# Optimization experiments

Measured on AMD Instinct MI355X. Metric: run time of the kernel, lower is better.

## Reference

```python
import jax, jax.numpy as jnp
import numpy as np

T, B, D, H, MID, A = 512, 128, 256, 512, 512, 3


def setup_inputs() -> dict:
    key = jax.random.key(0)
    ks = jax.random.split(key, 16)
    kb = 1.0 / np.sqrt(H)

    def u(kk, shape):
        return jax.random.uniform(kk, shape, jnp.float32, -kb, kb)

    def lin(kk, fan_in, fan_out, std=0.05):
        k1, k2 = jax.random.split(kk)
        return (jax.random.normal(k1, (fan_out, fan_in), jnp.float32) * std,
                jnp.full((fan_out,), 1e-6, jnp.float32))

    aw0, ab0 = lin(ks[6], H + D, MID)
    aw1, ab1 = lin(ks[7], MID, MID)
    aw2, ab2 = lin(ks[8], MID, A, std=0.1 / np.sqrt(MID))
    cw0, cb0 = lin(ks[9], H + D, MID)
    cw1, cb1 = lin(ks[10], MID, MID)
    cw2, cb2 = lin(ks[11], MID, 1, std=0.5 / np.sqrt(MID))

    return {
        "state": jax.random.normal(ks[0], (T, B, D), jnp.float32),
        "hidden_state": jnp.zeros((B, H), jnp.float32),
        "cell_state": jnp.zeros((B, H), jnp.float32),
        "len_sequence": jax.random.randint(ks[1], (B,), 1, T + 1),
        "W_ih": u(ks[2], (4 * H, D)), "W_hh": u(ks[3], (4 * H, H)),
        "b_ih": u(ks[4], (4 * H,)), "b_hh": u(ks[5], (4 * H,)),
        "aw0": aw0, "ab0": ab0, "aw1": aw1, "ab1": ab1, "aw2": aw2, "ab2": ab2,
        "cw0": cw0, "cb0": cb0, "cw1": cw1, "cb1": cb1, "cw2": cw2, "cb2": cb2,
    }


def _pack_indices(len_sequence):
    # ragged packing: concat first len[b] timesteps of each batch row
    lens = np.asarray(len_sequence)
    return jnp.asarray(np.concatenate(
        [b * T + np.arange(l) for b, l in enumerate(lens)]))


def _mlp(x, w0, b0, w1, b1, w2, b2):
    h = jax.nn.relu(x @ w0.T + b0)
    h = jax.nn.relu(h @ w1.T + b1)
    return h @ w2.T + b2


def reference(state, hidden_state, cell_state, len_sequence,
              W_ih, W_hh, b_ih, b_hh,
              aw0, ab0, aw1, ab1, aw2, ab2,
              cw0, cb0, cw1, cb1, cw2, cb2):
    flat_idx = _pack_indices(len_sequence)

    def step(carry, x_t):
        h, c = carry
        gates = x_t @ W_ih.T + b_ih + h @ W_hh.T + b_hh
        i, f, g, o = jnp.split(gates, 4, axis=-1)
        c = jax.nn.sigmoid(f) * c + jax.nn.sigmoid(i) * jnp.tanh(g)
        h = jax.nn.sigmoid(o) * jnp.tanh(c)
        return (h, c), h

    _, hs = jax.lax.scan(step, (hidden_state, cell_state), state)  # [T,B,H]

    rnn_emb = hs.transpose(1, 0, 2).reshape(B * T, H)[flat_idx]      # [N,H]
    st = state.transpose(1, 0, 2).reshape(B * T, D)[flat_idx]        # [N,D]
    inp = jnp.concatenate([st, rnn_emb], axis=1)                     # [N,D+H]

    actor = jnp.tanh(_mlp(inp, aw0, ab0, aw1, ab1, aw2, ab2))
    critic = _mlp(inp, cw0, cb0, cw1, cb1, cw2, cb2)
    return actor, critic
```

## Files before the change

### kernel.cpp

```cpp
#include <hip/hip_runtime.h>
#include <stdint.h>


#define T_STEPS 512
#define BATCH   128
#define DDIM    256
#define HDIM    512

typedef __attribute__((ext_vector_type(8))) short bf16x8;
typedef __attribute__((ext_vector_type(4))) float f32x4;
typedef __attribute__((ext_vector_type(2))) unsigned long long u64x2;
typedef unsigned short u16;
typedef unsigned int   u32;
typedef unsigned long long u64;
typedef __attribute__((ext_vector_type(4))) u32 u32x4;

__device__ __forceinline__ u16 f2bf(float x){
  u32 u = __builtin_bit_cast(u32, x);
  u32 r = u + 0x7fffu + ((u >> 16) & 1u);
  return (u16)(r >> 16);
}
__device__ __forceinline__ float bf2f(u16 h){
  u32 u = ((u32)h) << 16;
  return __builtin_bit_cast(float, u);
}
__device__ __forceinline__ float sigm(float x){ return 1.f/(1.f + __expf(-x)); }
__device__ __forceinline__ float tanh_f(float x){ return 1.f - 2.f/(1.f + __expf(2.f*x)); }

__device__ __forceinline__ void async_ld16(const void* g, void* l){
  __builtin_amdgcn_global_load_lds(
      (const __attribute__((address_space(1))) u32*)g,
      (__attribute__((address_space(3))) u32*)l, 16, 0, 0);
}

__device__ __forceinline__ void ld2_b128_cc_issue(const void* p0, const void* p1,
                                                  u32x4& A0, u32x4& A1){
  asm volatile("global_load_dwordx4 %0, %2, off sc0 sc1\n\t"
               "global_load_dwordx4 %1, %3, off sc0 sc1"
               : "=&v"(A0), "=&v"(A1) : "v"(p0), "v"(p1) : "memory");
}

__global__ void sniff_kernel(const u16* __restrict__ b, int* __restrict__ mode){
  if (threadIdx.x == 0){
    int bad = 0;
    for (int i = 0; i < 64; i++){
      u16 x = b[2*i];
      int e = (x >> 7) & 0xFF;
      if (e < 0x60 || e > 0x85) bad++;
    }
    *mode = (bad > 16) ? 1 : 0;
  }
}

__global__ void cvt_kernel(const void* __restrict__ src, u16* __restrict__ dst,
                           int n, const int* __restrict__ mode){
  int i0 = (blockIdx.x*blockDim.x + threadIdx.x) * 8;
  if (i0 >= n) return;
  int m = *mode;
  if (m){
    const float* s = (const float*)src;
    if (i0 + 8 <= n){
      float4 a = *(const float4*)(s + i0);
      float4 b = *(const float4*)(s + i0 + 4);
      ushort4 oa, ob;
      oa.x=f2bf(a.x); oa.y=f2bf(a.y); oa.z=f2bf(a.z); oa.w=f2bf(a.w);
      ob.x=f2bf(b.x); ob.y=f2bf(b.y); ob.z=f2bf(b.z); ob.w=f2bf(b.w);
      *(ushort4*)(dst + i0) = oa;
      *(ushort4*)(dst + i0 + 4) = ob;
    } else {
      for (int i = i0; i < n; i++) dst[i] = f2bf(s[i]);
    }
  } else {
    const u16* s = (const u16*)src;
    if (i0 + 8 <= n){
      *(ushort4*)(dst + i0)     = *(const ushort4*)(s + i0);
      *(ushort4*)(dst + i0 + 4) = *(const ushort4*)(s + i0 + 4);
    } else {
      for (int i = i0; i < n; i++) dst[i] = s[i];
    }
  }
}

__global__ void scan_kernel(const int* __restrict__ lens, int* __restrict__ off){
  if (threadIdx.x == 0){
    int a = 0;
    for (int b = 0; b < BATCH; b++){ off[b] = a; a += lens[b]; }
    off[BATCH] = a;
  }
}

__global__ void pack_state_kernel(const u16* __restrict__ st_bf,
                                  const int* __restrict__ lens,
                                  const int* __restrict__ off,
                                  u16* __restrict__ inp){
  int r = blockIdx.x*4 + (threadIdx.x >> 6);
  int lane = threadIdx.x & 63;
  int b = r & (BATCH-1), t = r >> 7;
  if (t >= lens[b]) return;
  long row = (long)off[b] + t;
  ushort4 v = ((const ushort4*)(st_bf + (long)r*DDIM))[lane];
  ((ushort4*)(inp + row*768))[lane] = v;
}

__global__ void zero_out_kernel(void* __restrict__ out, int n,
                                const int* __restrict__ mode){
  int i = blockIdx.x*blockDim.x + threadIdx.x;
  if (i >= n) return;
  if (*mode) ((float*)out)[i] = 0.f; else ((u16*)out)[i] = 0;
}

__global__ __launch_bounds__(512, 1) void lstm_kernel(
    const u16* __restrict__ Whh, const u16* __restrict__ Wih,
    const u16* __restrict__ bih, const u16* __restrict__ bhh,
    const u16* __restrict__ cell0,
    const u16* __restrict__ state,
    u16* hbuf,
    u16* __restrict__ inp,
    const int* __restrict__ off, const int* __restrict__ lens,
    int* tags)
{
  const int tid  = threadIdx.x;
  const int wave = tid >> 6;
  const int lane = tid & 63;
  const int g    = blockIdx.x >> 4;
  const int s    = blockIdx.x & 15;
  const int Sb   = s * 32;
  const int q    = lane >> 4;
  const int m16  = lane & 15;

  __shared__ u16  wlds[65536];
  __shared__ u16  hlds[8192];
  __shared__ float lds_acc[8][16][16];
  __shared__ float bias_l[128];
  __shared__ int   len_l[16];
  __shared__ int   off_l[16];

  if (tid < 128){
    int gt = tid >> 5, jx = tid & 31;
    int cg = gt*HDIM + Sb + jx;
    bias_l[tid] = bf2f(bih[cg]) + bf2f(bhh[cg]);
  }
  if (tid < 16){ len_l[tid] = lens[g*16 + tid]; off_l[tid] = off[g*16 + tid]; }

  for (int i = 0; i < 16; i++){
    int ch = tid + 512*i;
    int w = ch >> 10;
    int rem = ch & 1023;
    int c = rem >> 6;
    int l = rem & 63;
    int col = (w >> 1)*HDIM + Sb + (w & 1)*16 + (l & 15);
    int k = c*32 + (l >> 4)*8;
    u64x2 v = *(const u64x2*)(Whh + (long)col*HDIM + k);
    *(u64x2*)(&wlds[(size_t)ch*8]) = v;
  }

  const int gate = wave >> 1;
  const int hf   = wave & 1;
  const int colg = gate*HDIM + Sb + hf*16 + m16;
  bf16x8 wih[8];
  {
    const u16* wb2 = Wih + (long)colg*DDIM + q*8;
    #pragma unroll
    for (int c = 0; c < 8; c++) wih[c] = *(const bf16x8*)(wb2 + c*32);
  }

  const int b_l = tid >> 5;
  const int j   = tid & 31;
  const int hx  = j >> 4;
  const int jj  = j & 15;
  float cval = bf2f(cell0[(g*16 + b_l)*HDIM + Sb + j]);

  const int m0 = tid, m1 = tid + 512;
  const int c0i = m0 >> 6, c1i = m1 >> 6;
  const int r0 = m0 & 15;
  const int k0 = c0i*32 + ((m0 & 63) >> 4)*8;
  const int k1 = c1i*32 + ((m1 & 63) >> 4)*8;

  int* tg = tags + g*16;

  __syncthreads();

  for (int t = 0; t < T_STEPS; t++){
    f32x4 acc  = {0.f, 0.f, 0.f, 0.f};
    f32x4 acc2 = {0.f, 0.f, 0.f, 0.f};
    bf16x8 xa[8];
    {
      const u16* xb = state + ((long)(t*BATCH + g*16 + m16))*DDIM + q*8;
      #pragma unroll
      for (int c = 0; c < 8; c++) xa[c] = *(const bf16x8*)(xb + c*32);
    }
    if (t > 0){
      int spins = 0;
      for (;;){
        int tv = 0x7fffffff;
        if (lane < 16)
          tv = __hip_atomic_load(&tg[lane], __ATOMIC_RELAXED,
                                 __HIP_MEMORY_SCOPE_AGENT);
        if (__all(tv >= t)) break;
        if (++spins > (1 << 14)) break;
      }
      asm volatile("" ::: "memory");
    }
    const u16* hp = hbuf + ((t & 1) ^ 1)*(BATCH*HDIM) + (size_t)g*16*HDIM;
    u32x4 A0, A1;
    ld2_b128_cc_issue(hp + r0*HDIM + k0, hp + r0*HDIM + k1, A0, A1);
    #pragma unroll
    for (int c = 0; c < 8; c++)
      acc = __builtin_amdgcn_mfma_f32_16x16x32_bf16(xa[c], wih[c], acc, 0, 0, 0);
    asm volatile("s_waitcnt vmcnt(0)" ::: "memory");
    __builtin_amdgcn_sched_barrier(0);
    *(u32x4*)(&hlds[(size_t)m0*8]) = A0;
    *(u32x4*)(&hlds[(size_t)m1*8]) = A1;
    __syncthreads();
    #pragma unroll
    for (int cc = 0; cc < 8; cc++){
      bf16x8 a0 = *(const bf16x8*)(&hlds[(size_t)((2*cc    )*64 + lane)*8]);
      bf16x8 a1 = *(const bf16x8*)(&hlds[(size_t)((2*cc + 1)*64 + lane)*8]);
      bf16x8 w0 = *(const bf16x8*)(&wlds[(size_t)((wave*16 + 2*cc    )*64 + lane)*8]);
      bf16x8 w1 = *(const bf16x8*)(&wlds[(size_t)((wave*16 + 2*cc + 1)*64 + lane)*8]);
      acc  = __builtin_amdgcn_mfma_f32_16x16x32_bf16(a0, w0, acc,  0, 0, 0);
      acc2 = __builtin_amdgcn_mfma_f32_16x16x32_bf16(a1, w1, acc2, 0, 0, 0);
    }
    #pragma unroll
    for (int r = 0; r < 4; r++)
      lds_acc[wave][q*4 + r][m16] = acc[r] + acc2[r];
    __syncthreads();

    float iv = lds_acc[0 + hx][b_l][jj] + bias_l[ 0 + j];
    float fv = lds_acc[2 + hx][b_l][jj] + bias_l[32 + j];
    float gv = lds_acc[4 + hx][b_l][jj] + bias_l[64 + j];
    float ov = lds_acc[6 + hx][b_l][jj] + bias_l[96 + j];
    cval = sigm(fv)*cval + sigm(iv)*tanh_f(gv);
    float hv = sigm(ov)*tanh_f(cval);
    u16 hb16 = f2bf(hv);
    int nb = __shfl_down((int)hb16, 1);
    if ((j & 1) == 0){
      size_t hidx = (size_t)(t & 1)*(BATCH*HDIM) + (g*16 + b_l)*HDIM + Sb + j;
      u32 pair = (u32)hb16 | ((u32)(u16)nb << 16);
      __hip_atomic_store((u32*)(hbuf + hidx), pair,
                         __ATOMIC_RELAXED, __HIP_MEMORY_SCOPE_AGENT);
    }
    __builtin_amdgcn_s_waitcnt(0);
    __syncthreads();
    if (tid == 0)
      __hip_atomic_store(&tg[s], t + 1,
                         __ATOMIC_RELAXED, __HIP_MEMORY_SCOPE_AGENT);
    if (t < len_l[b_l])
      inp[((long)(off_l[b_l] + t))*768 + DDIM + Sb + j] = hb16;
  }
}

__global__ __launch_bounds__(256) void gemm_kernel(
    const u16* __restrict__ A,
    const u16* __restrict__ W,
    const u16* __restrict__ bias,
    u16* __restrict__ C,
    int K)
{
  __shared__ u16 As[128*32];
  __shared__ u16 Bs[128*32];
  const int tid = threadIdx.x, wave = tid >> 6, lane = tid & 63;
  const int bm = blockIdx.x * 128;
  const int bn = blockIdx.y * 128;
  const int wr = (wave >> 1) * 64;
  const int wc = (wave & 1) * 64;
  const int q = lane >> 4, m16 = lane & 15;
  const int rsub = lane >> 2;
  const int ksub = (lane & 3) * 8;

  f32x4 acc[4][4] = {};

  for (int k0 = 0; k0 < K; k0 += 32){
    __syncthreads();
    #pragma unroll
    for (int i = 0; i < 2; i++){
      int rr = (i*4 + wave) * 16 + rsub;
      async_ld16(A + (long)(bm + rr)*K + k0 + ksub, As + (i*4 + wave)*512);
      async_ld16(W + (long)(bn + rr)*K + k0 + ksub, Bs + (i*4 + wave)*512);
    }
    __syncthreads();
    bf16x8 af[4], bfr[4];
    #pragma unroll
    for (int r = 0; r < 4; r++) af[r]  = *(const bf16x8*)(As + (wr + r*16 + m16)*32 + q*8);
    #pragma unroll
    for (int c = 0; c < 4; c++) bfr[c] = *(const bf16x8*)(Bs + (wc + c*16 + m16)*32 + q*8);
    #pragma unroll
    for (int r = 0; r < 4; r++)
      #pragma unroll
      for (int c = 0; c < 4; c++)
        acc[r][c] = __builtin_amdgcn_mfma_f32_16x16x32_bf16(af[r], bfr[c], acc[r][c], 0, 0, 0);
  }
  #pragma unroll
  for (int c = 0; c < 4; c++){
    int col = bn + wc + c*16 + m16;
    float bv = bf2f(bias[col]);
    #pragma unroll
    for (int r = 0; r < 4; r++){
      #pragma unroll
      for (int x = 0; x < 4; x++){
        int row = bm + wr + r*16 + q*4 + x;
        float v = acc[r][c][x] + bv;
        v = fmaxf(v, 0.f);
        C[(long)row*512 + col] = f2bf(v);
      }
    }
  }
}

__global__ void final_kernel(
    const u16* __restrict__ a2, const u16* __restrict__ c2,
    const u16* __restrict__ aw2, const u16* __restrict__ ab2,
    const u16* __restrict__ cw2, const u16* __restrict__ cb2,
    void* __restrict__ out, int base, int nvalid, int N,
    const int* __restrict__ mode)
{
  int lw = (blockIdx.x * blockDim.x + threadIdx.x) >> 6;
  int lane = threadIdx.x & 63;
  if (lw >= nvalid) return;
  int k = lane * 8;
  bf16x8 av = *(const bf16x8*)(a2 + (long)lw*512 + k);
  bf16x8 cv = *(const bf16x8*)(c2 + (long)lw*512 + k);
  bf16x8 w0 = *(const bf16x8*)(aw2 + k);
  bf16x8 w1 = *(const bf16x8*)(aw2 + 512 + k);
  bf16x8 w2 = *(const bf16x8*)(aw2 + 1024 + k);
  bf16x8 wc = *(const bf16x8*)(cw2 + k);
  float d0=0.f, d1=0.f, d2=0.f, dc=0.f;
  #pragma unroll
  for (int x = 0; x < 8; x++){
    float a  = bf2f((u16)av[x]);
    float cc = bf2f((u16)cv[x]);
    d0 += a  * bf2f((u16)w0[x]);
    d1 += a  * bf2f((u16)w1[x]);
    d2 += a  * bf2f((u16)w2[x]);
    dc += cc * bf2f((u16)wc[x]);
  }
  #pragma unroll
  for (int o = 32; o > 0; o >>= 1){
    d0 += __shfl_down(d0, o);
    d1 += __shfl_down(d1, o);
    d2 += __shfl_down(d2, o);
    dc += __shfl_down(dc, o);
  }
  if (lane == 0){
    int gr = base + lw;
    float r0 = tanh_f(d0 + bf2f(ab2[0]));
    float r1 = tanh_f(d1 + bf2f(ab2[1]));
    float r2 = tanh_f(d2 + bf2f(ab2[2]));
    float rc = dc + bf2f(cb2[0]);
    if (*mode){
      float* o = (float*)out;
      o[(long)gr*3 + 0] = r0; o[(long)gr*3 + 1] = r1; o[(long)gr*3 + 2] = r2;
      o[(long)3*N + gr] = rc;
    } else {
      u16* o = (u16*)out;
      o[(long)gr*3 + 0] = f2bf(r0); o[(long)gr*3 + 1] = f2bf(r1);
      o[(long)gr*3 + 2] = f2bf(r2);
      o[(long)3*N + gr] = f2bf(rc);
    }
  }
}

extern "C" void kernel_launch(void* const* d_in, const int* in_sizes, int n_in,
                              void* d_out, int out_size, void* d_ws, size_t ws_size,
                              hipStream_t stream)
{
  const void* state = d_in[0];
  const void* h0    = d_in[1];
  const void* c0    = d_in[2];
  const int*  lens  = (const int*)d_in[3];
  const void* Wih   = d_in[4];
  const void* Whh   = d_in[5];
  const void* bih   = d_in[6];
  const void* bhh   = d_in[7];
  const void* aw0   = d_in[8];
  const void* ab0   = d_in[9];
  const void* aw1   = d_in[10];
  const void* ab1   = d_in[11];
  const void* aw2   = d_in[12];
  const void* ab2   = d_in[13];
  const void* cw0   = d_in[14];
  const void* cb0   = d_in[15];
  const void* cw1   = d_in[16];
  const void* cb1   = d_in[17];
  const void* cw2   = d_in[18];
  const void* cb2   = d_in[19];
  (void)in_sizes; (void)n_in;

  const int N = out_size / 4;
  const int Np128 = (N + 127) & ~127;

  char* ws = (char*)d_ws;
  size_t cur = 0;
  auto alloc = [&](size_t bytes)->char*{
    char* p = ws + cur; cur += (bytes + 255) & ~(size_t)255; return p;
  };
  int* mode   = (int*)alloc(4);
  int* off    = (int*)alloc(129*4);
  int* tags   = (int*)alloc(128*4);
  u16* hbuf   = (u16*)alloc((size_t)2*BATCH*HDIM*2);
  u16* cbf    = (u16*)alloc((size_t)BATCH*HDIM*2);
  u16* wih_b  = (u16*)alloc((size_t)2048*256*2);
  u16* whh_b  = (u16*)alloc((size_t)2048*512*2);
  u16* bih_b  = (u16*)alloc(2048*2);
  u16* bhh_b  = (u16*)alloc(2048*2);
  u16* st_bf  = (u16*)alloc((size_t)T_STEPS*BATCH*DDIM*2);
  u16* wa0    = (u16*)alloc((size_t)512*768*2);
  u16* ba0    = (u16*)alloc(512*2);
  u16* wa1    = (u16*)alloc((size_t)512*512*2);
  u16* ba1    = (u16*)alloc(512*2);
  u16* wa2    = (u16*)alloc(1536*2);
  u16* ba2    = (u16*)alloc(256*2);
  u16* wc0    = (u16*)alloc((size_t)512*768*2);
  u16* bc0    = (u16*)alloc(512*2);
  u16* wc1    = (u16*)alloc((size_t)512*512*2);
  u16* bc1    = (u16*)alloc(512*2);
  u16* wc2    = (u16*)alloc(512*2);
  u16* bc2    = (u16*)alloc(256*2);
  u16* inp    = (u16*)alloc((size_t)Np128*768*2);

  sniff_kernel<<<1, 64, 0, stream>>>((const u16*)bih, mode);

  if (cur > ws_size){
    zero_out_kernel<<<(out_size + 255)/256, 256, 0, stream>>>(d_out, out_size, mode);
    return;
  }
  size_t rem = ws_size - cur;
  long CH_l = (long)((rem / 3) / (512*2)) & ~127L;
  int CH = (int)(CH_l > 8192 ? 8192 : CH_l);
  if (CH < 128){
    zero_out_kernel<<<(out_size + 255)/256, 256, 0, stream>>>(d_out, out_size, mode);
    return;
  }
  u16* bufA = (u16*)alloc((size_t)CH*512*2);
  u16* bufB = (u16*)alloc((size_t)CH*512*2);
  u16* bufC = (u16*)alloc((size_t)CH*512*2);

  auto cvt = [&](const void* src, u16* dst, int n){
    int thr = (n + 7) / 8;
    cvt_kernel<<<(thr + 255)/256, 256, 0, stream>>>(src, dst, n, mode);
  };
  cvt(Wih, wih_b, 2048*256);
  cvt(Whh, whh_b, 2048*512);
  cvt(bih, bih_b, 2048);
  cvt(bhh, bhh_b, 2048);
  cvt(h0,  hbuf + BATCH*HDIM, BATCH*HDIM);
  cvt(c0,  cbf, BATCH*HDIM);
  cvt(state, st_bf, T_STEPS*BATCH*DDIM);
  cvt(aw0, wa0, 512*768);  cvt(ab0, ba0, 512);
  cvt(aw1, wa1, 512*512);  cvt(ab1, ba1, 512);
  cvt(aw2, wa2, 1536);     cvt(ab2, ba2, 3);
  cvt(cw0, wc0, 512*768);  cvt(cb0, bc0, 512);
  cvt(cw1, wc1, 512*512);  cvt(cb1, bc1, 512);
  cvt(cw2, wc2, 512);      cvt(cb2, bc2, 1);

  hipMemsetAsync(tags, 0, 128*4, stream);
  scan_kernel<<<1, 64, 0, stream>>>(lens, off);
  pack_state_kernel<<<(T_STEPS*BATCH)/4, 256, 0, stream>>>(st_bf, lens, off, inp);

  lstm_kernel<<<128, 512, 0, stream>>>(whh_b, wih_b, bih_b, bhh_b, cbf, st_bf,
                                       hbuf, inp, off, lens, tags);

  for (int cs = 0; cs < Np128; cs += CH){
    int rows = (Np128 - cs) < CH ? (Np128 - cs) : CH;
    int gm = rows / 128;
    dim3 gg(gm, 4);
    gemm_kernel<<<gg, 256, 0, stream>>>(inp + (long)cs*768, wa0, ba0, bufA, 768);
    gemm_kernel<<<gg, 256, 0, stream>>>(bufA,               wa1, ba1, bufB, 512);
    gemm_kernel<<<gg, 256, 0, stream>>>(inp + (long)cs*768, wc0, bc0, bufA, 768);
    gemm_kernel<<<gg, 256, 0, stream>>>(bufA,               wc1, bc1, bufC, 512);
    int nvalid = (N - cs) < rows ? (N - cs) : rows;
    if (nvalid > 0)
      final_kernel<<<(nvalid + 3)/4, 256, 0, stream>>>(bufB, bufC, wa2, ba2,
                                                       wc2, bc2, d_out, cs,
                                                       nvalid, N, mode);
  }
}
```

Measured before the change: 2.764 ms.

## Use XCD-local cache-scope sync when partner blocks share an XCD

Block-to-group mapping changes so that the 16 slice blocks of each batch group have blockIdx values congruent mod 8, which places them on the same XCD under round-robin dispatch. A startup probe then checks whether these partners can see each other's sc0 (L2-scope) stores. If they can, the per-step h exchange and tag polling use sc0 loads and stores instead of device-coherent sc1 or atomic accesses, which cuts the latency of each recurrent step. The risk is relying on an undocumented dispatch placement, plus extra startup synchronisation with a fallback path.

```diff
diff --git a/kernel.cpp b/kernel.cpp
--- a/kernel.cpp
+++ b/kernel.cpp
@@ -33,6 +33,22 @@
       (__attribute__((address_space(3))) u32*)l, 16, 0, 0);
 }
 
+__device__ __forceinline__ u32 ld_u32_sc0(const int* p){
+  u32 v;
+  asm volatile("global_load_dword %0, %1, off sc0\n\t"
+               "s_waitcnt vmcnt(0)"
+               : "=&v"(v) : "v"(p) : "memory");
+  return v;
+}
+__device__ __forceinline__ void st_u32_sc0(int* p, u32 v){
+  asm volatile("global_store_dword %0, %1, off sc0" :: "v"(p), "v"(v) : "memory");
+}
+__device__ __forceinline__ void ld2_b128_sc0_issue(const void* p0, const void* p1,
+                                                   u32x4& A0, u32x4& A1){
+  asm volatile("global_load_dwordx4 %0, %2, off sc0\n\t"
+               "global_load_dwordx4 %1, %3, off sc0"
+               : "=&v"(A0), "=&v"(A1) : "v"(p0), "v"(p1) : "memory");
+}
 __device__ __forceinline__ void ld2_b128_cc_issue(const void* p0, const void* p1,
                                                   u32x4& A0, u32x4& A1){
   asm volatile("global_load_dwordx4 %0, %2, off sc0 sc1\n\t"
@@ -117,13 +133,14 @@
     u16* hbuf,
     u16* __restrict__ inp,
     const int* __restrict__ off, const int* __restrict__ lens,
-    int* tags)
+    int* tags,
+    int* probe)
 {
   const int tid  = threadIdx.x;
   const int wave = tid >> 6;
   const int lane = tid & 63;
-  const int g    = blockIdx.x >> 4;
-  const int s    = blockIdx.x & 15;
+  const int g    = blockIdx.x & 7;
+  const int s    = blockIdx.x >> 3;
   const int Sb   = s * 32;
   const int q    = lane >> 4;
   const int m16  = lane & 15;
@@ -134,6 +151,46 @@
   __shared__ float bias_l[128];
   __shared__ int   len_l[16];
   __shared__ int   off_l[16];
+  __shared__ int   fast_l;
+
+  if (wave == 0){
+    if (lane == 0){
+      st_u32_sc0(&probe[blockIdx.x], 0xC0FFEE00u | (u32)blockIdx.x);
+      asm volatile("s_waitcnt vmcnt(0)" ::: "memory");
+      st_u32_sc0(&probe[128 + blockIdx.x], 1u);
+    }
+    int seen = 1;
+    if (lane < 16){
+      int partner = 8*lane + g;
+      seen = 0;
+      for (int sp = 0; sp < (1 << 11); sp++){
+        u32 tgv = ld_u32_sc0(&probe[128 + partner]);
+        if (tgv == 1u){
+          u32 v = ld_u32_sc0(&probe[partner]);
+          if (v == (0xC0FFEE00u | (u32)partner)) seen = 1;
+          break;
+        }
+      }
+    }
+    int okl = __all(seen != 0) ? 1 : 0;
+    if (lane == 0){
+      if (!okl)
+        __hip_atomic_fetch_or(&probe[256], 1,
+                              __ATOMIC_RELAXED, __HIP_MEMORY_SCOPE_AGENT);
+      __hip_atomic_fetch_add(&probe[257], 1,
+                             __ATOMIC_RELEASE, __HIP_MEMORY_SCOPE_AGENT);
+      int sp2 = 0;
+      while (__hip_atomic_load(&probe[257], __ATOMIC_ACQUIRE,
+                               __HIP_MEMORY_SCOPE_AGENT) < 128){
+        if (++sp2 >= (1 << 16)) break;
+      }
+      int bad = __hip_atomic_load(&probe[256], __ATOMIC_RELAXED,
+                                  __HIP_MEMORY_SCOPE_AGENT);
+      int cnt = __hip_atomic_load(&probe[257], __ATOMIC_RELAXED,
+                                  __HIP_MEMORY_SCOPE_AGENT);
+      fast_l = (!bad && cnt >= 128) ? 1 : 0;
+    }
+  }
 
   if (tid < 128){
     int gt = tid >> 5, jx = tid & 31;
@@ -179,6 +236,7 @@
   int* tg = tags + g*16;
 
   __syncthreads();
+  const int fast = fast_l;
 
   for (int t = 0; t < T_STEPS; t++){
     f32x4 acc  = {0.f, 0.f, 0.f, 0.f};
@@ -191,19 +249,29 @@
     }
     if (t > 0){
       int spins = 0;
-      for (;;){
-        int tv = 0x7fffffff;
-        if (lane < 16)
-          tv = __hip_atomic_load(&tg[lane], __ATOMIC_RELAXED,
-                                 __HIP_MEMORY_SCOPE_AGENT);
-        if (__all(tv >= t)) break;
-        if (++spins > (1 << 14)) break;
+      if (fast){
+        for (;;){
+          int tv = 0x7fffffff;
+          if (lane < 16) tv = (int)ld_u32_sc0(&tg[lane]);
+          if (__all(tv >= t)) break;
+          if (++spins > (1 << 14)) break;
+        }
+      } else {
+        for (;;){
+          int tv = 0x7fffffff;
+          if (lane < 16)
+            tv = __hip_atomic_load(&tg[lane], __ATOMIC_RELAXED,
+                                   __HIP_MEMORY_SCOPE_AGENT);
+          if (__all(tv >= t)) break;
+          if (++spins > (1 << 14)) break;
+        }
       }
       asm volatile("" ::: "memory");
     }
     const u16* hp = hbuf + ((t & 1) ^ 1)*(BATCH*HDIM) + (size_t)g*16*HDIM;
     u32x4 A0, A1;
-    ld2_b128_cc_issue(hp + r0*HDIM + k0, hp + r0*HDIM + k1, A0, A1);
+    if (fast) ld2_b128_sc0_issue(hp + r0*HDIM + k0, hp + r0*HDIM + k1, A0, A1);
+    else      ld2_b128_cc_issue (hp + r0*HDIM + k0, hp + r0*HDIM + k1, A0, A1);
     #pragma unroll
     for (int c = 0; c < 8; c++)
       acc = __builtin_amdgcn_mfma_f32_16x16x32_bf16(xa[c], wih[c], acc, 0, 0, 0);
@@ -237,14 +305,17 @@
     if ((j & 1) == 0){
       size_t hidx = (size_t)(t & 1)*(BATCH*HDIM) + (g*16 + b_l)*HDIM + Sb + j;
       u32 pair = (u32)hb16 | ((u32)(u16)nb << 16);
-      __hip_atomic_store((u32*)(hbuf + hidx), pair,
-                         __ATOMIC_RELAXED, __HIP_MEMORY_SCOPE_AGENT);
+      if (fast) st_u32_sc0((int*)(hbuf + hidx), pair);
+      else      __hip_atomic_store((u32*)(hbuf + hidx), pair,
+                                   __ATOMIC_RELAXED, __HIP_MEMORY_SCOPE_AGENT);
     }
     __builtin_amdgcn_s_waitcnt(0);
     __syncthreads();
-    if (tid == 0)
-      __hip_atomic_store(&tg[s], t + 1,
-                         __ATOMIC_RELAXED, __HIP_MEMORY_SCOPE_AGENT);
+    if (tid == 0){
+      if (fast) st_u32_sc0(&tg[s], (u32)(t + 1));
+      else      __hip_atomic_store(&tg[s], t + 1,
+                                   __ATOMIC_RELAXED, __HIP_MEMORY_SCOPE_AGENT);
+    }
     if (t < len_l[b_l])
       inp[((long)(off_l[b_l] + t))*768 + DDIM + Sb + j] = hb16;
   }
@@ -397,6 +468,7 @@
   int* mode   = (int*)alloc(4);
   int* off    = (int*)alloc(129*4);
   int* tags   = (int*)alloc(128*4);
+  int* probe  = (int*)alloc(512*4);
   u16* hbuf   = (u16*)alloc((size_t)2*BATCH*HDIM*2);
   u16* cbf    = (u16*)alloc((size_t)BATCH*HDIM*2);
   u16* wih_b  = (u16*)alloc((size_t)2048*256*2);
@@ -454,11 +526,12 @@
   cvt(cw2, wc2, 512);      cvt(cb2, bc2, 1);
 
   hipMemsetAsync(tags, 0, 128*4, stream);
+  hipMemsetAsync(probe, 0, 512*4, stream);
   scan_kernel<<<1, 64, 0, stream>>>(lens, off);
   pack_state_kernel<<<(T_STEPS*BATCH)/4, 256, 0, stream>>>(st_bf, lens, off, inp);
 
   lstm_kernel<<<128, 512, 0, stream>>>(whh_b, wih_b, bih_b, bhh_b, cbf, st_bf,
-                                       hbuf, inp, off, lens, tags);
+                                       hbuf, inp, off, lens, tags, probe);
 
   for (int cs = 0; cs < Np128; cs += CH){
     int rows = (Np128 - cs) < CH ? (Np128 - cs) : CH;
```

Result: faster. 2.409 ms (-12.8%).
